# Kernel tuning notes

Hardware: AMD Instinct MI355X
Metric: run time of the kernel (lower is better)

Reference implementation:

```python
import jax, jax.numpy as jnp
import numpy as np

FOCAL = 1015.0
IMG = 256


def setup_inputs() -> dict:
    key = jax.random.key(0)
    ks = jax.random.split(key, 9)
    B, NV, NF = 128, 35709, 70789
    coeff = jax.random.normal(ks[0], (B, 257), jnp.float32) * 0.1
    meanshape = jax.random.normal(ks[1], (NV * 3,), jnp.float32)
    idBase = jax.random.normal(ks[2], (NV * 3, 80), jnp.float32) * 0.01
    exBase = jax.random.normal(ks[3], (NV * 3, 64), jnp.float32) * 0.01
    meantex = jax.random.uniform(ks[4], (NV * 3,), jnp.float32) * 255.0
    texBase = jax.random.normal(ks[5], (NV * 3, 80), jnp.float32)
    # 1-based indices, matching the facemodel convention (code subtracts 1)
    tri = jax.random.randint(ks[6], (NF, 3), 1, NV + 1, jnp.int32)
    # point_buf may reference the appended zero face (index NF+1, 1-based)
    point_buf = jax.random.randint(ks[7], (NV, 8), 1, NF + 2, jnp.int32)
    kp_inds = jax.random.randint(ks[8], (68,), 0, NV, jnp.int32)
    return dict(coeff=coeff, meanshape=meanshape, idBase=idBase, exBase=exBase,
                meantex=meantex, texBase=texBase, tri=tri, point_buf=point_buf,
                kp_inds=kp_inds)


def _rotation(angles):
    # rotation = (Rz @ Ry @ Rx)^T, per Compute_rotation_matrix
    sx, sy, sz = jnp.sin(angles[:, 0]), jnp.sin(angles[:, 1]), jnp.sin(angles[:, 2])
    cx, cy, cz = jnp.cos(angles[:, 0]), jnp.cos(angles[:, 1]), jnp.cos(angles[:, 2])
    o, l = jnp.zeros_like(sx), jnp.ones_like(sx)
    Rx = jnp.stack([l, o, o, o, cx, -sx, o, sx, cx], -1).reshape(-1, 3, 3)
    Ry = jnp.stack([cy, o, sy, o, l, o, -sy, o, cy], -1).reshape(-1, 3, 3)
    Rz = jnp.stack([cz, -sz, o, sz, cz, o, o, o, l], -1).reshape(-1, 3, 3)
    return jnp.einsum('bij,bjk,bkl->bli', Rz, Ry, Rx)


def _compute_norm(shape, tri, point_buf):
    fid = tri - 1  # [F,3] 0-based vertex ids
    v1 = shape[:, fid[:, 0]]  # [B,F,3]
    v2 = shape[:, fid[:, 1]]
    v3 = shape[:, fid[:, 2]]
    fn = jnp.cross(v1 - v2, v2 - v3)  # per-face normals [B,F,3]
    fn = jnp.concatenate([fn, jnp.zeros_like(fn[:, :1])], axis=1)  # pad zero face
    vn = fn[:, point_buf - 1].sum(axis=2)  # [B,NV,8,3] -> [B,NV,3]
    return vn / jnp.linalg.norm(vn, axis=2, keepdims=True)


def _illumination(tex, norm, gamma):
    B, N, _ = tex.shape
    gamma = gamma.reshape(B, 3, 9).at[:, :, 0].add(0.8).transpose(0, 2, 1)  # [B,9,3]
    a0 = np.pi
    a1 = 2.0 * np.pi / np.sqrt(3.0)
    a2 = 2.0 * np.pi / np.sqrt(8.0)
    c0 = 1.0 / np.sqrt(4.0 * np.pi)
    c1 = np.sqrt(3.0) / np.sqrt(4.0 * np.pi)
    c2 = 3.0 * np.sqrt(5.0) / np.sqrt(12.0 * np.pi)
    d0 = 0.5 / np.sqrt(3.0)
    nx, ny, nz = norm[..., 0], norm[..., 1], norm[..., 2]
    Y = jnp.stack([
        jnp.full_like(nx, np.float32(a0 * c0)),
        -a1 * c1 * ny,
        a1 * c1 * nz,
        -a1 * c1 * nx,
        a2 * c2 * nx * ny,
        -a2 * c2 * ny * nz,
        a2 * c2 * d0 * (3.0 * nz ** 2 - 1.0),
        -a2 * c2 * nx * nz,
        a2 * c2 * 0.5 * (nx ** 2 - ny ** 2),
    ], axis=-1)  # [B,N,9]
    lighting = jnp.einsum('bnc,bcd->bnd', Y, gamma)  # [B,N,3]
    return tex * lighting


def _project(pts):
    half = IMG // 2
    pts = pts * jnp.array([1.0, 1.0, -1.0], jnp.float32) + jnp.array([0.0, 0.0, 10.0], jnp.float32)
    P = jnp.array([[FOCAL, 0.0, half], [0.0, FOCAL, half], [0.0, 0.0, 1.0]], jnp.float32)
    aug = pts @ P.T
    return aug[..., :2] / aug[..., 2:3]


def reference(coeff, meanshape, idBase, exBase, meantex, texBase, tri, point_buf, kp_inds):
    B = coeff.shape[0]
    idc, exc, texc = coeff[:, :80], coeff[:, 80:144], coeff[:, 144:224]
    angles, gamma, trans = coeff[:, 224:227], coeff[:, 227:254], coeff[:, 254:257]
    # Shape_formation
    shape = (idc @ idBase.T + exc @ exBase.T + meanshape).reshape(B, -1, 3)
    shape = shape - meanshape.reshape(1, -1, 3).mean(axis=1, keepdims=True)
    # Texture_formation
    tex = (texc @ texBase.T + meantex).reshape(B, -1, 3)
    # Normals, rotation, rigid transform
    vnorm = _compute_norm(shape, tri, point_buf)
    rot = _rotation(angles)  # [B,3,3]
    vnorm_r = jnp.einsum('bnc,bcd->bnd', vnorm, rot)
    shape_t = jnp.einsum('bnc,bcd->bnd', shape, rot) + trans[:, None, :]
    # Illumination (vertex colors) and landmark projection
    face_color = _illumination(tex, vnorm_r, gamma)
    lms = _project(shape_t[:, kp_inds])
    lms = jnp.stack([lms[..., 0], IMG - lms[..., 1]], axis=-1)
    return face_color, lms, shape_t
```

## Files before the change

kernel.cpp:

```cpp
#include <hip/hip_runtime.h>

typedef unsigned short u16;
typedef unsigned int u32;
typedef __attribute__((ext_vector_type(8))) short bfrag;
typedef __attribute__((ext_vector_type(4))) float ffrag;
typedef __attribute__((ext_vector_type(4))) float f4;
typedef __attribute__((ext_vector_type(2))) float f2;
typedef __attribute__((ext_vector_type(4))) int i4;
typedef __attribute__((ext_vector_type(4))) _Float16 h4;

#define NVERT 35709
#define NFACE 70789
#define NV3   107127
#define NB    128

#define SHAPE_OFF 0ull
#define TEX_OFF   54849024ull
#define FQ_OFF    82273536ull
#define CPACK_OFF 154761472ull
#define MPAD_OFF  154827008ull
#define GG_OFF    154833152ull
#define MEAN_OFF  154846976ull
#define PART_OFF  154846992ull

#define LMS_BASE  13712256ull
#define ST_BASE   13729664ull

__device__ __forceinline__ float b2f(u16 s) {
  union { unsigned u; float f; } v; v.u = ((unsigned)s) << 16; return v.f;
}
__device__ __forceinline__ u16 f2b(float x) {
  union { float f; unsigned u; } v; v.f = x;
  unsigned r = v.u + 0x7FFFu + ((v.u >> 16) & 1u);
  return (u16)(r >> 16);
}
__device__ __forceinline__ f4 ld4u(const float* p) {
  f4 r; __builtin_memcpy(&r, p, 16); return r;
}
__device__ __forceinline__ bfrag cvt8nt(const float* p) {
  f4 a = __builtin_nontemporal_load((const f4*)p);
  f4 b = __builtin_nontemporal_load((const f4*)(p + 4));
  bfrag r;
  r[0] = (short)f2b(a.x); r[1] = (short)f2b(a.y); r[2] = (short)f2b(a.z); r[3] = (short)f2b(a.w);
  r[4] = (short)f2b(b.x); r[5] = (short)f2b(b.y); r[6] = (short)f2b(b.z); r[7] = (short)f2b(b.w);
  return r;
}

__global__ __launch_bounds__(256) void k_mean(const float* __restrict__ ms, float* __restrict__ part) {
  __shared__ float s[3];
  if (threadIdx.x < 3) s[threadIdx.x] = 0.f;
  __syncthreads();
  float a0 = 0.f, a1 = 0.f, a2 = 0.f;
  for (int v = blockIdx.x * 256 + threadIdx.x; v < NVERT; v += 64 * 256) {
    a0 += ms[v * 3 + 0];
    a1 += ms[v * 3 + 1];
    a2 += ms[v * 3 + 2];
  }
  atomicAdd(&s[0], a0); atomicAdd(&s[1], a1); atomicAdd(&s[2], a2);
  __syncthreads();
  if (threadIdx.x < 3) part[blockIdx.x * 3 + threadIdx.x] = s[threadIdx.x];
}

__global__ __launch_bounds__(128) void k_params(const float* __restrict__ coeff, u16* __restrict__ cpack,
                                                float* __restrict__ mpad, float* __restrict__ G,
                                                const float* __restrict__ part, float* __restrict__ mean) {
  int b = threadIdx.x;
  if (b < 3) {
    float s = 0.f;
    for (int i = 0; i < 64; i++) s += part[i * 3 + b];
    mean[b] = s * (1.0f / (float)NVERT);
  }
  const float* c = coeff + b * 257;
  u16* cp = cpack + b * 256;
  for (int k = 0; k < 80; k++) cp[k] = f2b(c[k]);
  for (int k = 80; k < 96; k++) cp[k] = 0;
  for (int k = 0; k < 64; k++) cp[96 + k] = f2b(c[80 + k]);
  for (int k = 0; k < 80; k++) cp[160 + k] = f2b(c[144 + k]);
  for (int k = 240; k < 256; k++) cp[k] = 0;
  float ax = c[224], ay = c[225], az = c[226];
  float sx = sinf(ax), cx = cosf(ax);
  float sy = sinf(ay), cy = cosf(ay);
  float sz = sinf(az), cz = cosf(az);
  float* mp = mpad + b * 12;
  mp[0] = cz * cy;  mp[1] = cz * sy * sx - sz * cx;  mp[2] = sz * sx + cz * sy * cx;
  mp[3] = sz * cy;  mp[4] = cz * cx + sz * sy * sx;  mp[5] = sz * sy * cx - cz * sx;
  mp[6] = -sy;      mp[7] = cy * sx;                 mp[8] = cy * cx;
  mp[9] = c[254]; mp[10] = c[255]; mp[11] = c[256];
  float* g = G + b * 27;
  for (int cc = 0; cc < 9; cc++)
    for (int d = 0; d < 3; d++)
      g[cc * 3 + d] = c[227 + d * 9 + cc] + (cc == 0 ? 0.8f : 0.0f);
}

#define SBLK 558
__global__ __launch_bounds__(256) void k_gemmS(const float* __restrict__ idB, const float* __restrict__ exB,
                                               const float* __restrict__ ms, const u16* __restrict__ cpack,
                                               const float* __restrict__ meanc, const float* __restrict__ mpad,
                                               float* __restrict__ shp, float* __restrict__ out) {
  __shared__ float SW[4][2][384];
  int wave = threadIdx.x >> 6, lane = threadIdx.x & 63;
  int col = lane & 15, quad = lane >> 4;
  int jb = (blockIdx.x * 4 + wave) * 48;
  bfrag z8 = {0, 0, 0, 0, 0, 0, 0, 0};
  bfrag bid[3][3], bex[3][2];
  float msj[3], mcv[3];
#pragma unroll
  for (int T = 0; T < 3; T++) {
    int j = jb + T * 16 + col;
    int jc = j < NV3 ? j : NV3 - 1;
    const float* rowI = idB + (size_t)jc * 80;
    const float* rowE = exB + (size_t)jc * 64;
#pragma unroll
    for (int f = 0; f < 3; f++) {
      int k = f * 32 + quad * 8;
      bool ok = (k < 80);
      int ks = ok ? k : 0;
      bfrag vi = cvt8nt(rowI + ks);
      bid[T][f] = ok ? vi : z8;
    }
#pragma unroll
    for (int f = 0; f < 2; f++) bex[T][f] = cvt8nt(rowE + f * 32 + quad * 8);
    msj[T] = ms[jc];
    mcv[T] = meanc[jc % 3];
  }
  float (*SWl)[384] = SW[wave];
  int s0 = quad >> 1;
  int rb = (quad & 1) << 2;
  int vb = jb / 3;
  int ilim = NV3 - jb; ilim = (ilim > 48 ? 48 : ilim) * 8;
  int vlim = NVERT - vb; vlim = vlim > 16 ? 16 : vlim;

  for (int bt = 0; bt < 8; bt++) {
    const u16* cp = cpack + (size_t)(bt * 16 + col) * 256;
#pragma unroll
    for (int T = 0; T < 3; T++) {
      ffrag acc = {0.f, 0.f, 0.f, 0.f};
#pragma unroll
      for (int f = 0; f < 3; f++) {
        bfrag a = *(const bfrag*)(cp + f * 32 + quad * 8);
        acc = __builtin_amdgcn_mfma_f32_16x16x32_bf16(a, bid[T][f], acc, 0, 0, 0);
      }
#pragma unroll
      for (int f = 0; f < 2; f++) {
        bfrag a = *(const bfrag*)(cp + 96 + f * 32 + quad * 8);
        acc = __builtin_amdgcn_mfma_f32_16x16x32_bf16(a, bex[T][f], acc, 0, 0, 0);
      }
#pragma unroll
      for (int rr = 0; rr < 2; rr++) {
        f2 v2;
        v2.x = acc[2 * rr] + msj[T] - mcv[T];
        v2.y = acc[2 * rr + 1] + msj[T] - mcv[T];
        *(f2*)&SWl[s0][(T * 16 + col) * 8 + rb + 2 * rr] = v2;
      }
    }
#pragma unroll
    for (int s = 0; s < 2; s++) {
      size_t sb = (size_t)(bt * 2 + s) * (size_t)(NV3 * 8) + (size_t)jb * 8;
#pragma unroll
      for (int it = 0; it < 3; it++) {
        int i = it * 128 + lane * 2;
        if (i < ilim) {
          f2 vv = *(f2*)&SWl[s][i];
          __builtin_nontemporal_store(vv, (f2*)(shp + sb + i));
        }
      }
    }
#pragma unroll
    for (int s = 0; s < 2; s++) {
#pragma unroll
      for (int kk = 0; kk < 2; kk++) {
        int bi = (lane >> 4) + (kk << 2);
        int vloc = lane & 15;
        int b = bt * 16 + s * 8 + bi;
        float x = SWl[s][vloc * 24 + bi];
        float y = SWl[s][vloc * 24 + 8 + bi];
        float z = SWl[s][vloc * 24 + 16 + bi];
        const float* mp = mpad + b * 12;
        f4 m0 = *(const f4*)mp;
        f4 m1 = *(const f4*)(mp + 4);
        f4 m2 = *(const f4*)(mp + 8);
        if (vloc < vlim) {
          float ox = x * m0.x + y * m0.y + z * m0.z + m2.y;
          float oy = x * m0.w + y * m1.x + z * m1.y + m2.z;
          float oz = x * m1.z + y * m1.w + z * m2.x + m2.w;
          size_t o = ST_BASE + (size_t)b * NV3 + (size_t)(vb + vloc) * 3;
          __builtin_nontemporal_store(ox, out + o);
          __builtin_nontemporal_store(oy, out + o + 1);
          __builtin_nontemporal_store(oz, out + o + 2);
        }
      }
    }
  }
}

__global__ __launch_bounds__(256) void k_gemmT(const float* __restrict__ txB, const float* __restrict__ mt,
                                               const u16* __restrict__ cpack, u16* __restrict__ texo) {
  __shared__ u32 tT[4][128];
  int wave = threadIdx.x >> 6, lane = threadIdx.x & 63;
  int jt = blockIdx.x * 4 + wave;
  int col = lane & 15, quad = lane >> 4;
  int j = jt * 16 + col;
  int jc = j < NV3 ? j : NV3 - 1;
  bfrag z8 = {0, 0, 0, 0, 0, 0, 0, 0};
  bfrag btx[3];
  const float* rowT = txB + (size_t)jc * 80;
#pragma unroll
  for (int f = 0; f < 3; f++) {
    int k = f * 32 + quad * 8;
    bool ok = (k < 80);
    int ks = ok ? k : 0;
    bfrag vt = cvt8nt(rowT + ks);
    btx[f] = ok ? vt : z8;
  }
  float mtj = mt[jc];
  u32* tw = &tT[wave][0];
  int slot = (quad >> 1) * 64 + col * 4 + (quad & 1) * 2;

  for (int bt = 0; bt < 8; bt++) {
    const u16* cp = cpack + (size_t)(bt * 16 + col) * 256;
    ffrag accT = {0.f, 0.f, 0.f, 0.f};
#pragma unroll
    for (int f = 0; f < 3; f++) {
      bfrag a = *(const bfrag*)(cp + 160 + f * 32 + quad * 8);
      accT = __builtin_amdgcn_mfma_f32_16x16x32_bf16(a, btx[f], accT, 0, 0, 0);
    }
#pragma unroll
    for (int rr = 0; rr < 2; rr++)
      tw[slot + rr] = (u32)f2b(accT[2 * rr] + mtj) | ((u32)f2b(accT[2 * rr + 1] + mtj) << 16);
#pragma unroll
    for (int s2 = 0; s2 < 2; s2++) {
      int o = lane << 1;
      int j2 = jt * 16 + (o >> 3);
      if (j2 < NV3) {
        size_t sb = (size_t)(bt * 2 + s2) * (size_t)(NV3 * 8);
        u32 tv = tT[wave][s2 * 64 + lane];
        __builtin_nontemporal_store(tv, (u32*)(texo + sb + (size_t)(jt * 128 + o)));
      }
    }
  }
}

#define FN_CH2 2213
__global__ __launch_bounds__(256) void k_fn(const float* __restrict__ shpT, const int* __restrict__ tri,
                                            h4* __restrict__ fq) {
  int g = blockIdx.x;
  int xcd = g & 7, sgi = g >> 3;
  int btg = sgi / FN_CH2, chunk = sgi - btg * FN_CH2;
  int bt8 = btg * 8 + xcd;
  int t = threadIdx.x;
  int bi = t & 7, foff = t >> 3;
  int f = chunk * 32 + foff;
  if (f >= NFACE) return;
  int i0 = tri[f * 3 + 0] - 1;
  int i1 = tri[f * 3 + 1] - 1;
  int i2 = tri[f * 3 + 2] - 1;
  const float* sl = shpT + (size_t)bt8 * (size_t)(NV3 * 8);
  int a0 = i0 * 24 + bi, a1 = i1 * 24 + bi, a2 = i2 * 24 + bi;
  float x1 = sl[a0], y1 = sl[a0 + 8], z1 = sl[a0 + 16];
  float x2 = sl[a1], y2 = sl[a1 + 8], z2 = sl[a1 + 16];
  float x3 = sl[a2], y3 = sl[a2 + 8], z3 = sl[a2 + 16];
  float e1x = x1 - x2, e1y = y1 - y2, e1z = z1 - z2;
  float e2x = x2 - x3, e2y = y2 - y3, e2z = z2 - z3;
  h4 st;
  st.x = (_Float16)(e1y * e2z - e1z * e2y);
  st.y = (_Float16)(e1z * e2x - e1x * e2z);
  st.z = (_Float16)(e1x * e2y - e1y * e2x);
  st.w = (_Float16)0.f;
  fq[(size_t)bt8 * (size_t)(NFACE * 8) + (size_t)f * 8 + bi] = st;
}

#define FI_CH2 1116
__global__ __launch_bounds__(256) void k_final(const u16* __restrict__ texT, const h4* __restrict__ fq,
                                               const int* __restrict__ pbuf, const float* __restrict__ mpad,
                                               const float* __restrict__ G, float* __restrict__ out) {
  __shared__ float scol[8][100];
  int g = blockIdx.x;
  int xcd = g & 7, sgi = g >> 3;
  int btg = sgi / FI_CH2, chunk = sgi - btg * FI_CH2;
  int bt8 = btg * 8 + xcd;
  int t = threadIdx.x;
  int bi = t & 7, voff = t >> 3;
  int v0 = chunk * 32;
  int v = v0 + voff;
  int vc = v < NVERT ? v : NVERT - 1;
  bool valid = v < NVERT;
  int b = bt8 * 8 + bi;
  i4 p0 = *(const i4*)(pbuf + (size_t)vc * 8);
  i4 p1 = *(const i4*)(pbuf + (size_t)vc * 8 + 4);
  int idx[8] = {p0.x, p0.y, p0.z, p0.w, p1.x, p1.y, p1.z, p1.w};
  const h4* fb = fq + (size_t)bt8 * (size_t)(NFACE * 8);
  float vx = 0.f, vy = 0.f, vz = 0.f;
#pragma unroll
  for (int i = 0; i < 8; i++) {
    int id = idx[i] - 1;
    if (id < NFACE) {
      h4 q = fb[(size_t)id * 8 + bi];
      vx += (float)q.x; vy += (float)q.y; vz += (float)q.z;
    }
  }
  float n2 = vx * vx + vy * vy + vz * vz;
  float inv = rsqrtf(fmaxf(n2, 1e-30f));
  vx *= inv; vy *= inv; vz *= inv;
  const float* mp = mpad + b * 12;
  f4 m0 = *(const f4*)mp;
  f4 m1 = *(const f4*)(mp + 4);
  float m8 = mp[8];
  float nx = vx * m0.x + vy * m0.y + vz * m0.z;
  float ny = vx * m0.w + vy * m1.x + vz * m1.y;
  float nz = vx * m1.z + vy * m1.w + vz * m8;
  const float kc1 = 1.7724539f;
  const float kc2 = 2.4270324f;
  const float kd0 = 0.28867513f;
  float Y[9];
  Y[0] = 0.8862269f;
  Y[1] = -kc1 * ny;
  Y[2] = kc1 * nz;
  Y[3] = -kc1 * nx;
  Y[4] = kc2 * nx * ny;
  Y[5] = -kc2 * ny * nz;
  Y[6] = kc2 * kd0 * (3.f * nz * nz - 1.f);
  Y[7] = -kc2 * nx * nz;
  Y[8] = kc2 * 0.5f * (nx * nx - ny * ny);
  const float* gg = G + b * 27;
  float gv[28];
#pragma unroll
  for (int q = 0; q < 7; q++) {
    f4 g4 = ld4u(gg + q * 4);
    gv[q * 4] = g4.x; gv[q * 4 + 1] = g4.y; gv[q * 4 + 2] = g4.z; gv[q * 4 + 3] = g4.w;
  }
  const u16* tp = texT + (size_t)bt8 * (size_t)(NV3 * 8) + (size_t)vc * 24 + bi;
  if (valid) {
#pragma unroll
    for (int d = 0; d < 3; d++) {
      float L = 0.f;
#pragma unroll
      for (int cc = 0; cc < 9; cc++) L += Y[cc] * gv[cc * 3 + d];
      float tx = b2f(__builtin_nontemporal_load(tp + d * 8));
      scol[bi][voff * 3 + d] = tx * L;
    }
  }
  __syncthreads();
  int nvv = NVERT - v0;
  int lim = (nvv < 32 ? nvv : 32) * 3;
  size_t base = (size_t)(bt8 * 8) * NV3 + (size_t)v0 * 3;
#pragma unroll
  for (int it = 0; it < 3; it++) {
    int l = it * 256 + t;
    int b2 = l / 96, e = l - b2 * 96;
    if (e < lim) {
      size_t o = base + (size_t)b2 * NV3 + e;
      __builtin_nontemporal_store(scol[b2][e], out + o);
    }
  }
}

__global__ __launch_bounds__(128) void k_lms(const float* __restrict__ shpT, const int* __restrict__ kp,
                                             const float* __restrict__ mpad, float* __restrict__ out) {
  int t = threadIdx.x;
  int b = blockIdx.x;
  if (t >= 68) return;
  int v = kp[t];
  const float* sl = shpT + (size_t)(b >> 3) * (size_t)(NV3 * 8) + (size_t)v * 24 + (b & 7);
  float sx = sl[0], sy = sl[8], sz = sl[16];
  const float* mp = mpad + b * 12;
  f4 m0 = *(const f4*)mp;
  f4 m1 = *(const f4*)(mp + 4);
  f4 m2 = *(const f4*)(mp + 8);
  float ox = sx * m0.x + sy * m0.y + sz * m0.z + m2.y;
  float oy = sx * m0.w + sy * m1.x + sz * m1.y + m2.z;
  float oz = sx * m1.z + sy * m1.w + sz * m2.x + m2.w;
  float w = 10.f - oz;
  float invw = 1.0f / w;
  float lx = 1015.f * ox * invw + 128.f;
  float ly = 1015.f * oy * invw + 128.f;
  size_t o = LMS_BASE + ((size_t)b * 68 + t) * 2;
  out[o + 0] = lx;
  out[o + 1] = 256.f - ly;
}

extern "C" void kernel_launch(void* const* d_in, const int* in_sizes, int n_in,
                              void* d_out, int out_size, void* d_ws, size_t ws_size,
                              hipStream_t stream) {
  const float* coeff     = (const float*)d_in[0];
  const float* meanshape = (const float*)d_in[1];
  const float* idB       = (const float*)d_in[2];
  const float* exB       = (const float*)d_in[3];
  const float* meantex   = (const float*)d_in[4];
  const float* txB       = (const float*)d_in[5];
  const int* tri         = (const int*)d_in[6];
  const int* pbuf        = (const int*)d_in[7];
  const int* kp          = (const int*)d_in[8];
  float* out = (float*)d_out;
  char* ws = (char*)d_ws;
  float* shpT = (float*)(ws + SHAPE_OFF);
  u16* texT   = (u16*)(ws + TEX_OFF);
  h4* fq      = (h4*)(ws + FQ_OFF);
  u16* cpack  = (u16*)(ws + CPACK_OFF);
  float* mpad = (float*)(ws + MPAD_OFF);
  float* G    = (float*)(ws + GG_OFF);
  float* mean = (float*)(ws + MEAN_OFF);
  float* part = (float*)(ws + PART_OFF);

  k_mean<<<64, 256, 0, stream>>>(meanshape, part);
  k_params<<<1, 128, 0, stream>>>(coeff, cpack, mpad, G, part, mean);
  k_gemmS<<<SBLK, 256, 0, stream>>>(idB, exB, meanshape, cpack, mean, mpad, shpT, out);
  k_gemmT<<<1674, 256, 0, stream>>>(txB, meantex, cpack, texT);
  k_fn<<<8 * 2 * FN_CH2, 256, 0, stream>>>(shpT, tri, fq);
  k_final<<<8 * 2 * FI_CH2, 256, 0, stream>>>(texT, fq, pbuf, mpad, G, out);
  k_lms<<<128, 128, 0, stream>>>(shpT, kp, mpad, out);
}
```

Measured before the change: 420.1 us.

## Repack texture and face-normal buffers, split fn/final into two cache-sized passes

The texture GEMM output is re-laid out so each vertex's three channels for a batch lane sit in one 8-byte word, which k_final reads with a single vector load. Face normals are split from padded half4 into an xy u32 array and a separate z u16 array, cutting the fourth unused component. k_fn and k_final now run as two interleaved launches over half the batch-tile groups each, so the face-normal data for one half stays cache-resident before it is gathered. The cost is more kernel launches, more LDS traffic in gemmT, and two separate gathers per face instead of one.

```diff
diff --git a/kernel.cpp b/kernel.cpp
--- a/kernel.cpp
+++ b/kernel.cpp
@@ -6,8 +6,8 @@
 typedef __attribute__((ext_vector_type(4))) float ffrag;
 typedef __attribute__((ext_vector_type(4))) float f4;
 typedef __attribute__((ext_vector_type(2))) float f2;
+typedef __attribute__((ext_vector_type(2))) u32 u32x2;
 typedef __attribute__((ext_vector_type(4))) int i4;
-typedef __attribute__((ext_vector_type(4))) _Float16 h4;
 
 #define NVERT 35709
 #define NFACE 70789
@@ -15,13 +15,14 @@
 #define NB    128
 
 #define SHAPE_OFF 0ull
-#define TEX_OFF   54849024ull
-#define FQ_OFF    82273536ull
-#define CPACK_OFF 154761472ull
-#define MPAD_OFF  154827008ull
-#define GG_OFF    154833152ull
-#define MEAN_OFF  154846976ull
-#define PART_OFF  154846992ull
+#define TEX4_OFF  54849024ull
+#define FXY_OFF   91415040ull
+#define FZ_OFF    127659008ull
+#define CPACK_OFF 145780992ull
+#define MPAD_OFF  145846528ull
+#define GG_OFF    145852672ull
+#define MEAN_OFF  145866496ull
+#define PART_OFF  145866512ull
 
 #define LMS_BASE  13712256ull
 #define ST_BASE   13729664ull
@@ -33,6 +34,12 @@
   union { float f; unsigned u; } v; v.f = x;
   unsigned r = v.u + 0x7FFFu + ((v.u >> 16) & 1u);
   return (u16)(r >> 16);
+}
+__device__ __forceinline__ u16 h2b(float x) {
+  union { _Float16 h; u16 u; } v; v.h = (_Float16)x; return v.u;
+}
+__device__ __forceinline__ float hb2f(u16 u) {
+  union { _Float16 h; u16 u2; } v; v.u2 = u; return (float)v.h;
 }
 __device__ __forceinline__ f4 ld4u(const float* p) {
   f4 r; __builtin_memcpy(&r, p, 16); return r;
@@ -194,47 +201,67 @@
 }
 
 __global__ __launch_bounds__(256) void k_gemmT(const float* __restrict__ txB, const float* __restrict__ mt,
-                                               const u16* __restrict__ cpack, u16* __restrict__ texo) {
-  __shared__ u32 tT[4][128];
+                                               const u16* __restrict__ cpack, u32* __restrict__ tex4) {
+  __shared__ u16 TW[4][2][384];
   int wave = threadIdx.x >> 6, lane = threadIdx.x & 63;
-  int jt = blockIdx.x * 4 + wave;
   int col = lane & 15, quad = lane >> 4;
-  int j = jt * 16 + col;
-  int jc = j < NV3 ? j : NV3 - 1;
+  int jb = (blockIdx.x * 4 + wave) * 48;
   bfrag z8 = {0, 0, 0, 0, 0, 0, 0, 0};
-  bfrag btx[3];
-  const float* rowT = txB + (size_t)jc * 80;
-#pragma unroll
-  for (int f = 0; f < 3; f++) {
-    int k = f * 32 + quad * 8;
-    bool ok = (k < 80);
-    int ks = ok ? k : 0;
-    bfrag vt = cvt8nt(rowT + ks);
-    btx[f] = ok ? vt : z8;
-  }
-  float mtj = mt[jc];
-  u32* tw = &tT[wave][0];
-  int slot = (quad >> 1) * 64 + col * 4 + (quad & 1) * 2;
+  bfrag btx[3][3];
+  float mtj[3];
+#pragma unroll
+  for (int T = 0; T < 3; T++) {
+    int j = jb + T * 16 + col;
+    int jc = j < NV3 ? j : NV3 - 1;
+    const float* rowT = txB + (size_t)jc * 80;
+#pragma unroll
+    for (int f = 0; f < 3; f++) {
+      int k = f * 32 + quad * 8;
+      bool ok = (k < 80);
+      int ks = ok ? k : 0;
+      bfrag vt = cvt8nt(rowT + ks);
+      btx[T][f] = ok ? vt : z8;
+    }
+    mtj[T] = mt[jc];
+  }
+  u16 (*TWl)[384] = TW[wave];
+  int s0 = quad >> 1;
+  int rb = (quad & 1) << 2;
+  int vb = jb / 3;
+  int vlim = NVERT - vb; vlim = vlim > 16 ? 16 : vlim;
 
   for (int bt = 0; bt < 8; bt++) {
     const u16* cp = cpack + (size_t)(bt * 16 + col) * 256;
-    ffrag accT = {0.f, 0.f, 0.f, 0.f};
-#pragma unroll
-    for (int f = 0; f < 3; f++) {
-      bfrag a = *(const bfrag*)(cp + 160 + f * 32 + quad * 8);
-      accT = __builtin_amdgcn_mfma_f32_16x16x32_bf16(a, btx[f], accT, 0, 0, 0);
-    }
-#pragma unroll
-    for (int rr = 0; rr < 2; rr++)
-      tw[slot + rr] = (u32)f2b(accT[2 * rr] + mtj) | ((u32)f2b(accT[2 * rr + 1] + mtj) << 16);
-#pragma unroll
-    for (int s2 = 0; s2 < 2; s2++) {
-      int o = lane << 1;
-      int j2 = jt * 16 + (o >> 3);
-      if (j2 < NV3) {
-        size_t sb = (size_t)(bt * 2 + s2) * (size_t)(NV3 * 8);
-        u32 tv = tT[wave][s2 * 64 + lane];
-        __builtin_nontemporal_store(tv, (u32*)(texo + sb + (size_t)(jt * 128 + o)));
+#pragma unroll
+    for (int T = 0; T < 3; T++) {
+      ffrag acc = {0.f, 0.f, 0.f, 0.f};
+#pragma unroll
+      for (int f = 0; f < 3; f++) {
+        bfrag a = *(const bfrag*)(cp + 160 + f * 32 + quad * 8);
+        acc = __builtin_amdgcn_mfma_f32_16x16x32_bf16(a, btx[T][f], acc, 0, 0, 0);
+      }
+#pragma unroll
+      for (int rr = 0; rr < 2; rr++) {
+        TWl[s0][(T * 16 + col) * 8 + rb + 2 * rr]     = f2b(acc[2 * rr] + mtj[T]);
+        TWl[s0][(T * 16 + col) * 8 + rb + 2 * rr + 1] = f2b(acc[2 * rr + 1] + mtj[T]);
+      }
+    }
+#pragma unroll
+    for (int s = 0; s < 2; s++) {
+#pragma unroll
+      for (int kk = 0; kk < 2; kk++) {
+        int bi = (lane >> 4) + (kk << 2);
+        int vloc = lane & 15;
+        if (vloc < vlim) {
+          u16 x = TWl[s][(vloc * 3 + 0) * 8 + bi];
+          u16 y = TWl[s][(vloc * 3 + 1) * 8 + bi];
+          u16 z = TWl[s][(vloc * 3 + 2) * 8 + bi];
+          u32x2 val;
+          val.x = (u32)x | ((u32)y << 16);
+          val.y = (u32)z;
+          size_t idx = (((size_t)(bt * 2 + s) * NVERT + (vb + vloc)) * 8 + bi) * 2;
+          __builtin_nontemporal_store(val, (u32x2*)(tex4 + idx));
+        }
       }
     }
   }
@@ -242,11 +269,10 @@
 
 #define FN_CH2 2213
 __global__ __launch_bounds__(256) void k_fn(const float* __restrict__ shpT, const int* __restrict__ tri,
-                                            h4* __restrict__ fq) {
+                                            u32* __restrict__ fxy, u16* __restrict__ fz, int lo) {
   int g = blockIdx.x;
-  int xcd = g & 7, sgi = g >> 3;
-  int btg = sgi / FN_CH2, chunk = sgi - btg * FN_CH2;
-  int bt8 = btg * 8 + xcd;
+  int xcd = g & 7, chunk = g >> 3;
+  int bt8 = lo + xcd;
   int t = threadIdx.x;
   int bi = t & 7, foff = t >> 3;
   int f = chunk * 32 + foff;
@@ -261,23 +287,23 @@
   float x3 = sl[a2], y3 = sl[a2 + 8], z3 = sl[a2 + 16];
   float e1x = x1 - x2, e1y = y1 - y2, e1z = z1 - z2;
   float e2x = x2 - x3, e2y = y2 - y3, e2z = z2 - z3;
-  h4 st;
-  st.x = (_Float16)(e1y * e2z - e1z * e2y);
-  st.y = (_Float16)(e1z * e2x - e1x * e2z);
-  st.z = (_Float16)(e1x * e2y - e1y * e2x);
-  st.w = (_Float16)0.f;
-  fq[(size_t)bt8 * (size_t)(NFACE * 8) + (size_t)f * 8 + bi] = st;
+  u16 hx = h2b(e1y * e2z - e1z * e2y);
+  u16 hy = h2b(e1z * e2x - e1x * e2z);
+  u16 hz = h2b(e1x * e2y - e1y * e2x);
+  size_t o = (size_t)bt8 * (size_t)(NFACE * 8) + (size_t)f * 8 + bi;
+  fxy[o] = (u32)hx | ((u32)hy << 16);
+  fz[o] = hz;
 }
 
 #define FI_CH2 1116
-__global__ __launch_bounds__(256) void k_final(const u16* __restrict__ texT, const h4* __restrict__ fq,
-                                               const int* __restrict__ pbuf, const float* __restrict__ mpad,
-                                               const float* __restrict__ G, float* __restrict__ out) {
+__global__ __launch_bounds__(256) void k_final(const u32* __restrict__ tex4, const u32* __restrict__ fxy,
+                                               const u16* __restrict__ fz, const int* __restrict__ pbuf,
+                                               const float* __restrict__ mpad, const float* __restrict__ G,
+                                               float* __restrict__ out, int lo) {
   __shared__ float scol[8][100];
   int g = blockIdx.x;
-  int xcd = g & 7, sgi = g >> 3;
-  int btg = sgi / FI_CH2, chunk = sgi - btg * FI_CH2;
-  int bt8 = btg * 8 + xcd;
+  int xcd = g & 7, chunk = g >> 3;
+  int bt8 = lo + xcd;
   int t = threadIdx.x;
   int bi = t & 7, voff = t >> 3;
   int v0 = chunk * 32;
@@ -288,14 +314,16 @@
   i4 p0 = *(const i4*)(pbuf + (size_t)vc * 8);
   i4 p1 = *(const i4*)(pbuf + (size_t)vc * 8 + 4);
   int idx[8] = {p0.x, p0.y, p0.z, p0.w, p1.x, p1.y, p1.z, p1.w};
-  const h4* fb = fq + (size_t)bt8 * (size_t)(NFACE * 8);
+  const u32* fx = fxy + (size_t)bt8 * (size_t)(NFACE * 8);
+  const u16* fzb = fz + (size_t)bt8 * (size_t)(NFACE * 8);
   float vx = 0.f, vy = 0.f, vz = 0.f;
 #pragma unroll
   for (int i = 0; i < 8; i++) {
     int id = idx[i] - 1;
     if (id < NFACE) {
-      h4 q = fb[(size_t)id * 8 + bi];
-      vx += (float)q.x; vy += (float)q.y; vz += (float)q.z;
+      u32 q = fx[(size_t)id * 8 + bi];
+      u16 qz = fzb[(size_t)id * 8 + bi];
+      vx += hb2f((u16)q); vy += hb2f((u16)(q >> 16)); vz += hb2f(qz);
     }
   }
   float n2 = vx * vx + vy * vy + vz * vz;
@@ -328,15 +356,16 @@
     f4 g4 = ld4u(gg + q * 4);
     gv[q * 4] = g4.x; gv[q * 4 + 1] = g4.y; gv[q * 4 + 2] = g4.z; gv[q * 4 + 3] = g4.w;
   }
-  const u16* tp = texT + (size_t)bt8 * (size_t)(NV3 * 8) + (size_t)vc * 24 + bi;
   if (valid) {
+    u32x2 tv = __builtin_nontemporal_load(
+        (const u32x2*)(tex4 + ((size_t)bt8 * NVERT + vc) * 16 + bi * 2));
+    float tc[3] = { b2f((u16)tv.x), b2f((u16)(tv.x >> 16)), b2f((u16)tv.y) };
 #pragma unroll
     for (int d = 0; d < 3; d++) {
       float L = 0.f;
 #pragma unroll
       for (int cc = 0; cc < 9; cc++) L += Y[cc] * gv[cc * 3 + d];
-      float tx = b2f(__builtin_nontemporal_load(tp + d * 8));
-      scol[bi][voff * 3 + d] = tx * L;
+      scol[bi][voff * 3 + d] = tc[d] * L;
     }
   }
   __syncthreads();
@@ -393,8 +422,9 @@
   float* out = (float*)d_out;
   char* ws = (char*)d_ws;
   float* shpT = (float*)(ws + SHAPE_OFF);
-  u16* texT   = (u16*)(ws + TEX_OFF);
-  h4* fq      = (h4*)(ws + FQ_OFF);
+  u32* tex4   = (u32*)(ws + TEX4_OFF);
+  u32* fxy    = (u32*)(ws + FXY_OFF);
+  u16* fzp    = (u16*)(ws + FZ_OFF);
   u16* cpack  = (u16*)(ws + CPACK_OFF);
   float* mpad = (float*)(ws + MPAD_OFF);
   float* G    = (float*)(ws + GG_OFF);
@@ -404,8 +434,10 @@
   k_mean<<<64, 256, 0, stream>>>(meanshape, part);
   k_params<<<1, 128, 0, stream>>>(coeff, cpack, mpad, G, part, mean);
   k_gemmS<<<SBLK, 256, 0, stream>>>(idB, exB, meanshape, cpack, mean, mpad, shpT, out);
-  k_gemmT<<<1674, 256, 0, stream>>>(txB, meantex, cpack, texT);
-  k_fn<<<8 * 2 * FN_CH2, 256, 0, stream>>>(shpT, tri, fq);
-  k_final<<<8 * 2 * FI_CH2, 256, 0, stream>>>(texT, fq, pbuf, mpad, G, out);
+  k_gemmT<<<SBLK, 256, 0, stream>>>(txB, meantex, cpack, tex4);
+  for (int lo = 0; lo < 16; lo += 8) {
+    k_fn<<<8 * FN_CH2, 256, 0, stream>>>(shpT, tri, fxy, fzp, lo);
+    k_final<<<8 * FI_CH2, 256, 0, stream>>>(tex4, fxy, fzp, pbuf, mpad, G, out, lo);
+  }
   k_lms<<<128, 128, 0, stream>>>(shpT, kp, mpad, out);
 }
```

New measurement: 434.4 us. 3.4% more time.
